# Kernel optimization log

Hardware: AMD Instinct MI355X
Metric: run time of the kernel (lower is better)

Reference implementation:

```python
import jax, jax.numpy as jnp
import numpy as np

# SMPL-style skeleton: parent index per joint (parent < child, root = -1)
PARENTS = [-1, 0, 0, 0, 1, 2, 3, 4, 5, 6, 7, 8, 9, 9, 9, 12, 13, 14, 16, 17, 18, 19, 20, 21]
END_SITES = [10, 11, 15, 22, 23]  # feet, head, hands
NUM_JOINTS = len(PARENTS)


def rot6d_to_matrix(x):
    """6D rotation rep -> 3x3 matrix via Gram-Schmidt. x: [..., 6] -> [..., 3, 3].
    eye(3).reshape(-1)[:6] = [1,0,0,0,1,0] maps to identity under this (row-stacked) convention."""
    a1, a2 = x[..., 0:3], x[..., 3:6]
    b1 = a1 / jnp.linalg.norm(a1, axis=-1, keepdims=True)
    a2p = a2 - jnp.sum(b1 * a2, axis=-1, keepdims=True) * b1
    b2 = a2p / jnp.linalg.norm(a2p, axis=-1, keepdims=True)
    b3 = jnp.cross(b1, b2)
    return jnp.stack([b1, b2, b3], axis=-2)


def fk_positions(rot, offsets):
    """Forward kinematics (faithful to _recompute_joint_global_info).
    rot: [F, J, 3, 3] local joint rotations; offsets: [F, J, 3].
    Returns global joint positions [F, J, 3]. Loop is over the fixed, small
    joint hierarchy (structural), fully vectorized over frames."""
    positions = [offsets[:, 0]]          # root: offset only
    orientations = [rot[:, 0]]           # root: local rotation
    for i in range(1, NUM_JOINTS):
        pi = PARENTS[i]
        po = orientations[pi]            # [F, 3, 3]
        pos = jnp.einsum('fab,fb->fa', po, offsets[:, i]) + positions[pi]
        positions.append(pos)
        orientations.append(po @ rot[:, i])
    return jnp.stack(positions, axis=1)  # [F, J, 3]


def setup_inputs() -> dict:
    key = jax.random.key(0)
    ks = jax.random.split(key, 6)
    F = 65536
    return {
        'poseA': jax.random.normal(ks[0], (F, NUM_JOINTS, 6), dtype=jnp.float32),
        'poseB': jax.random.normal(ks[1], (F, NUM_JOINTS, 6), dtype=jnp.float32),
        'joint_offsets_A': jax.random.normal(ks[2], (F, NUM_JOINTS, 3), dtype=jnp.float32),
        'joint_offsets_B': jax.random.normal(ks[3], (F, NUM_JOINTS, 3), dtype=jnp.float32),
        't_poseA': jax.random.normal(ks[4], (NUM_JOINTS, 3), dtype=jnp.float32),
        't_poseB': jax.random.normal(ks[5], (NUM_JOINTS, 3), dtype=jnp.float32),
    }


def reference(poseA, poseB, joint_offsets_A, joint_offsets_B, t_poseA, t_poseB):
    ee = jnp.array(END_SITES)
    # 6D -> rotation matrices (to_matrix)
    RA = rot6d_to_matrix(poseA)
    RB = rot6d_to_matrix(poseB)
    # sequential per-joint FK (the hot loop)
    posA = fk_positions(RA, joint_offsets_A)
    posB = fk_positions(RB, joint_offsets_B)
    # bbox scale from T-pose
    scale_A = jnp.max(t_poseA, axis=0) - jnp.min(t_poseA, axis=0)  # [3]
    scale_B = jnp.max(t_poseB, axis=0) - jnp.min(t_poseB, axis=0)
    eeA = posA[:, ee, :] - t_poseA[ee, :]   # [F, E, 3]
    eeB = posB[:, ee, :] - t_poseB[ee, :]
    loss = jnp.mean((eeA / scale_A - eeB / scale_B) ** 2)
    return loss
```

## Files before the change

kernel.cpp:

```cpp
#include <hip/hip_runtime.h>


struct V3 { float x, y, z; };
struct M3 { float m[3][3]; };
struct FK { M3 o; V3 p; };

__device__ __forceinline__ V3 matvec(const M3& A, const V3& v) {
    return { A.m[0][0]*v.x + A.m[0][1]*v.y + A.m[0][2]*v.z,
             A.m[1][0]*v.x + A.m[1][1]*v.y + A.m[1][2]*v.z,
             A.m[2][0]*v.x + A.m[2][1]*v.y + A.m[2][2]*v.z };
}

__device__ __forceinline__ M3 matmul(const M3& A, const M3& B) {
    M3 C;
#pragma unroll
    for (int i = 0; i < 3; i++)
#pragma unroll
        for (int j = 0; j < 3; j++)
            C.m[i][j] = A.m[i][0]*B.m[0][j] + A.m[i][1]*B.m[1][j] + A.m[i][2]*B.m[2][j];
    return C;
}

__device__ __forceinline__ M3 rot6d(float v0, float v1, float v2,
                                    float v3, float v4, float v5) {
    float n1 = v0*v0 + v1*v1 + v2*v2;
    float r1 = 1.0f / sqrtf(n1);
    V3 b1 = { v0*r1, v1*r1, v2*r1 };
    float d = b1.x*v3 + b1.y*v4 + b1.z*v5;
    V3 u = { v3 - d*b1.x, v4 - d*b1.y, v5 - d*b1.z };
    float n2 = u.x*u.x + u.y*u.y + u.z*u.z;
    float r2 = 1.0f / sqrtf(n2);
    V3 b2 = { u.x*r2, u.y*r2, u.z*r2 };
    V3 b3 = { b1.y*b2.z - b1.z*b2.y, b1.z*b2.x - b1.x*b2.z, b1.x*b2.y - b1.y*b2.x };
    M3 R;
    R.m[0][0]=b1.x; R.m[0][1]=b1.y; R.m[0][2]=b1.z;
    R.m[1][0]=b2.x; R.m[1][1]=b2.y; R.m[1][2]=b2.z;
    R.m[2][0]=b3.x; R.m[2][1]=b3.y; R.m[2][2]=b3.z;
    return R;
}

__device__ __forceinline__ FK fk_step(float a0,float a1,float a2,float a3,float a4,float a5,
                                      float ox,float oy,float oz, const FK& par) {
    V3 t = matvec(par.o, {ox, oy, oz});
    FK s;
    s.p = { par.p.x + t.x, par.p.y + t.y, par.p.z + t.z };
    s.o = matmul(par.o, rot6d(a0, a1, a2, a3, a4, a5));
    return s;
}

__device__ __forceinline__ V3 fk_end(float ox, float oy, float oz, const FK& par) {
    V3 t = matvec(par.o, {ox, oy, oz});
    return { par.p.x + t.x, par.p.y + t.y, par.p.z + t.z };
}

#define GLDS16(gp, lp) __builtin_amdgcn_global_load_lds( \
    (const __attribute__((address_space(1))) void*)(gp), \
    (__attribute__((address_space(3))) void*)(lp), 16, 0, 0)

#define VWAIT(n) do { asm volatile("s_waitcnt vmcnt(" #n ")" ::: "memory"); \
                      __builtin_amdgcn_sched_barrier(0); } while (0)
#define LWAIT0()  do { asm volatile("s_waitcnt lgkmcnt(0)" ::: "memory"); \
                      __builtin_amdgcn_sched_barrier(0); } while (0)

__device__ __forceinline__ void stage(const float* __restrict__ P,
                                      const float* __restrict__ O,
                                      const int* pOfs, const int* oOfs,
                                      float4* pbuf, float4* obuf, int st) {
#pragma unroll
    for (int k = 0; k < 6; k++)
        GLDS16(P + st*24 + pOfs[k], pbuf + 64*k);
#pragma unroll
    for (int k = 0; k < 3; k++)
        GLDS16(O + st*12 + oOfs[k], obuf + 64*k);
}

#define READQ(pb, ob) \
    q0 = (pb)[0]; q1 = (pb)[1]; q2 = (pb)[2]; q3 = (pb)[3]; q4 = (pb)[4]; q5 = (pb)[5]; \
    r0 = (ob)[0]; r1 = (ob)[1]; r2 = (ob)[2];
#define J0ROT  q0.x,q0.y,q0.z,q0.w,q1.x,q1.y
#define J1ROT  q1.z,q1.w,q2.x,q2.y,q2.z,q2.w
#define J2ROT  q3.x,q3.y,q3.z,q3.w,q4.x,q4.y
#define J3ROT  q4.z,q4.w,q5.x,q5.y,q5.z,q5.w
#define J0OFF  r0.x,r0.y,r0.z
#define J1OFF  r0.w,r1.x,r1.y
#define J2OFF  r1.z,r1.w,r2.x
#define J3OFF  r2.y,r2.z,r2.w

__global__ __launch_bounds__(128)
void ee_loss_kernel(const float* __restrict__ poseA, const float* __restrict__ poseB,
                    const float* __restrict__ offA,  const float* __restrict__ offB,
                    const float* __restrict__ tA,    const float* __restrict__ tB,
                    float* __restrict__ out, float inv_count) {
    __shared__ float4 s_pose[2][2][64*6];
    __shared__ float4 s_off [2][2][64*3];
    __shared__ float s_inv[6];
    __shared__ float s_d[15];
    float* s_eeB = (float*)&s_off[0][0][0];

    const int tid  = threadIdx.x;
    const int wid  = tid >> 6;
    const int lane = tid & 63;
    const bool isB = wid & 1;
    const long long f0 = (long long)blockIdx.x * 64;

    const float* __restrict__ P = (isB ? poseB : poseA) + f0 * 144;
    const float* __restrict__ O = (isB ? offB  : offA ) + f0 * 72;

    float4* pb0 = &s_pose[wid][0][0];
    float4* pb1 = &s_pose[wid][1][0];
    float4* ob0 = &s_off[wid][0][0];
    float4* ob1 = &s_off[wid][1][0];
    const float4* rp0 = pb0 + lane * 6;
    const float4* rp1 = pb1 + lane * 6;
    const float4* ro0 = ob0 + lane * 3;
    const float4* ro1 = ob1 + lane * 3;

    if (tid < 6) {
        const float* tp = (tid < 3) ? tA : tB;
        int ax = (tid < 3) ? tid : tid - 3;
        float mn = tp[ax], mx = mn;
#pragma unroll
        for (int j = 1; j < 24; j++) {
            float v = tp[j*3 + ax];
            mn = fminf(mn, v); mx = fmaxf(mx, v);
        }
        s_inv[tid] = 1.0f / (mx - mn);
    }
    if (tid < 15) {
        const int EE[5] = {10, 11, 15, 22, 23};
        int e = tid / 3, ax = tid - 3*e;
        int j = EE[e];
        float mnA = tA[ax], mxA = mnA, mnB = tB[ax], mxB = mnB;
#pragma unroll
        for (int k = 1; k < 24; k++) {
            float a = tA[k*3 + ax], b = tB[k*3 + ax];
            mnA = fminf(mnA, a); mxA = fmaxf(mxA, a);
            mnB = fminf(mnB, b); mxB = fmaxf(mxB, b);
        }
        s_d[tid] = tB[j*3 + ax]/(mxB - mnB) - tA[j*3 + ax]/(mxA - mnA);
    }

    int pOfs[6], oOfs[3];
#pragma unroll
    for (int k = 0; k < 6; k++) {
        int idx = lane + 64*k, f = idx/6, c = idx - 6*f;
        pOfs[k] = f*144 + c*4;
    }
#pragma unroll
    for (int k = 0; k < 3; k++) {
        int idx = lane + 64*k, f = idx/3, c = idx - 3*f;
        oOfs[k] = f*72 + c*4;
    }

    stage(P, O, pOfs, oOfs, pb0, ob0, 0);
    stage(P, O, pOfs, oOfs, pb1, ob1, 1);

    float4 q0, q1, q2, q3, q4, q5, r0, r1, r2;

    VWAIT(9);
    READQ(rp0, ro0);
    LWAIT0();
    stage(P, O, pOfs, oOfs, pb0, ob0, 2);
    FK s0; s0.o = rot6d(J0ROT); s0.p = { r0.x, r0.y, r0.z };
    FK s1 = fk_step(J1ROT, J1OFF, s0);
    FK s2 = fk_step(J2ROT, J2OFF, s0);
    FK s3 = fk_step(J3ROT, J3OFF, s0);

    VWAIT(9);
    READQ(rp1, ro1);
    LWAIT0();
    stage(P, O, pOfs, oOfs, pb1, ob1, 3);
    FK s4 = fk_step(J0ROT, J0OFF, s1);
    FK s5 = fk_step(J1ROT, J1OFF, s2);
    FK s6 = fk_step(J2ROT, J2OFF, s3);
    FK s7 = fk_step(J3ROT, J3OFF, s4);

    VWAIT(9);
    READQ(rp0, ro0);
    LWAIT0();
    stage(P, O, pOfs, oOfs, pb0, ob0, 4);
    FK s8 = fk_step(J0ROT, J0OFF, s5);
    FK s9 = fk_step(J1ROT, J1OFF, s6);
    V3 e10 = fk_end(J2OFF, s7);
    V3 e11 = fk_end(J3OFF, s8);

    VWAIT(9);
    READQ(rp1, ro1);
    LWAIT0();
    stage(P, O, pOfs, oOfs, pb1, ob1, 5);
    FK s12 = fk_step(J0ROT, J0OFF, s9);
    FK s13 = fk_step(J1ROT, J1OFF, s9);
    FK s14 = fk_step(J2ROT, J2OFF, s9);
    V3 e15 = fk_end(J3OFF, s12);

    VWAIT(9);
    READQ(rp0, ro0);
    FK s16 = fk_step(J0ROT, J0OFF, s13);
    FK s17 = fk_step(J1ROT, J1OFF, s14);
    FK s18 = fk_step(J2ROT, J2OFF, s16);
    FK s19 = fk_step(J3ROT, J3OFF, s17);

    VWAIT(0);
    READQ(rp1, ro1);
    FK s20 = fk_step(J0ROT, J0OFF, s18);
    FK s21 = fk_step(J1ROT, J1OFF, s19);
    V3 e22 = fk_end(J2OFF, s20);
    V3 e23 = fk_end(J3OFF, s21);

    __syncthreads();
    if (isB) {
        float* eb = s_eeB + lane * 15;
        eb[ 0] = e10.x; eb[ 1] = e10.y; eb[ 2] = e10.z;
        eb[ 3] = e11.x; eb[ 4] = e11.y; eb[ 5] = e11.z;
        eb[ 6] = e15.x; eb[ 7] = e15.y; eb[ 8] = e15.z;
        eb[ 9] = e22.x; eb[10] = e22.y; eb[11] = e22.z;
        eb[12] = e23.x; eb[13] = e23.y; eb[14] = e23.z;
    }
    __syncthreads();

    if (!isB) {
        const float iax = s_inv[0], iay = s_inv[1], iaz = s_inv[2];
        const float ibx = s_inv[3], iby = s_inv[4], ibz = s_inv[5];
        const float* eb = s_eeB + lane * 15;
        float t0  = e10.x*iax - eb[ 0]*ibx + s_d[ 0];
        float t1  = e10.y*iay - eb[ 1]*iby + s_d[ 1];
        float t2  = e10.z*iaz - eb[ 2]*ibz + s_d[ 2];
        float t3  = e11.x*iax - eb[ 3]*ibx + s_d[ 3];
        float t4  = e11.y*iay - eb[ 4]*iby + s_d[ 4];
        float t5  = e11.z*iaz - eb[ 5]*ibz + s_d[ 5];
        float t6  = e15.x*iax - eb[ 6]*ibx + s_d[ 6];
        float t7  = e15.y*iay - eb[ 7]*iby + s_d[ 7];
        float t8  = e15.z*iaz - eb[ 8]*ibz + s_d[ 8];
        float t9  = e22.x*iax - eb[ 9]*ibx + s_d[ 9];
        float t10 = e22.y*iay - eb[10]*iby + s_d[10];
        float t11 = e22.z*iaz - eb[11]*ibz + s_d[11];
        float t12 = e23.x*iax - eb[12]*ibx + s_d[12];
        float t13 = e23.y*iay - eb[13]*iby + s_d[13];
        float t14 = e23.z*iaz - eb[14]*ibz + s_d[14];
        float local = ((t0*t0 + t1*t1) + (t2*t2 + t3*t3) + (t4*t4 + t5*t5) +
                       (t6*t6 + t7*t7) + (t8*t8 + t9*t9) + (t10*t10 + t11*t11) +
                       (t12*t12 + t13*t13) + t14*t14) * inv_count;
#pragma unroll
        for (int off = 32; off > 0; off >>= 1)
            local += __shfl_down(local, off, 64);
        if (lane == 0) atomicAdd(out, local);
    }
}

extern "C" void kernel_launch(void* const* d_in, const int* in_sizes, int n_in,
                              void* d_out, int out_size, void* d_ws, size_t ws_size,
                              hipStream_t stream) {
    const float* poseA = (const float*)d_in[0];
    const float* poseB = (const float*)d_in[1];
    const float* offA  = (const float*)d_in[2];
    const float* offB  = (const float*)d_in[3];
    const float* tA    = (const float*)d_in[4];
    const float* tB    = (const float*)d_in[5];
    float* out = (float*)d_out;

    const int F = in_sizes[0] / 144;
    const int blocks = F / 64;
    const float inv_count = 1.0f / ((float)F * 15.0f);

    hipMemsetAsync(out, 0, sizeof(float), stream);
    ee_loss_kernel<<<blocks, 128, 0, stream>>>(poseA, poseB, offA, offB, tA, tB,
                                               out, inv_count);
}
```

Measured before the change: 149.9 us.

## Pack A and B frames into one wave, exchange end-effectors via cross-half shuffle

Restructures the kernel so each 64-lane wave processes 32 frames, with the lower half computing skeleton A and the upper half skeleton B, instead of a 128-thread block with one wave per skeleton. The shared-memory round-trip and two __syncthreads used to combine A and B end-effectors are replaced by __shfl_xor across the wave halves. LDS reads are split into smaller groups interleaved with the FK steps to cut register pressure and overlap LDS latency. The price is twice as many blocks, half-wave-interleaved LDS layouts, and more waitcnt points. Half of each wave also sits idle during the loss arithmetic.

```diff
diff --git a/kernel.cpp b/kernel.cpp
--- a/kernel.cpp
+++ b/kernel.cpp
@@ -62,21 +62,24 @@
 #define LWAIT0()  do { asm volatile("s_waitcnt lgkmcnt(0)" ::: "memory"); \
                       __builtin_amdgcn_sched_barrier(0); } while (0)
 
-__device__ __forceinline__ void stage(const float* __restrict__ P,
-                                      const float* __restrict__ O,
-                                      const int* pOfs, const int* oOfs,
-                                      float4* pbuf, float4* obuf, int st) {
-#pragma unroll
-    for (int k = 0; k < 6; k++)
-        GLDS16(P + st*24 + pOfs[k], pbuf + 64*k);
-#pragma unroll
-    for (int k = 0; k < 3; k++)
-        GLDS16(O + st*12 + oOfs[k], obuf + 64*k);
-}
-
-#define READQ(pb, ob) \
-    q0 = (pb)[0]; q1 = (pb)[1]; q2 = (pb)[2]; q3 = (pb)[3]; q4 = (pb)[4]; q5 = (pb)[5]; \
-    r0 = (ob)[0]; r1 = (ob)[1]; r2 = (ob)[2];
+#define STAGE(B, ST) do { \
+    GLDS16(psrc[0] + (ST)*24, &s_pose[B][  0]); \
+    GLDS16(psrc[1] + (ST)*24, &s_pose[B][ 64]); \
+    GLDS16(psrc[2] + (ST)*24, &s_pose[B][128]); \
+    GLDS16(psrc[3] + (ST)*24, &s_pose[B][192]); \
+    GLDS16(psrc[4] + (ST)*24, &s_pose[B][256]); \
+    GLDS16(psrc[5] + (ST)*24, &s_pose[B][320]); \
+    GLDS16(osrc[0] + (ST)*12, &s_off [B][  0]); \
+    GLDS16(osrc[1] + (ST)*12, &s_off [B][ 64]); \
+    GLDS16(osrc[2] + (ST)*12, &s_off [B][128]); \
+} while (0)
+
+#define RG1(B)  q0 = s_pose[B][ps[0]]; q1 = s_pose[B][ps[1]]; q2 = s_pose[B][ps[2]]; \
+                r0 = s_off[B][os3[0]]; r1 = s_off[B][os3[1]];
+#define RQ35(B) q3 = s_pose[B][ps[3]]; q4 = s_pose[B][ps[4]]; q5 = s_pose[B][ps[5]];
+#define RQ34(B) q3 = s_pose[B][ps[3]]; q4 = s_pose[B][ps[4]];
+#define RR2(B)  r2 = s_off[B][os3[2]];
+
 #define J0ROT  q0.x,q0.y,q0.z,q0.w,q1.x,q1.y
 #define J1ROT  q1.z,q1.w,q2.x,q2.y,q2.z,q2.w
 #define J2ROT  q3.x,q3.y,q3.z,q3.w,q4.x,q4.y
@@ -86,49 +89,38 @@
 #define J2OFF  r1.z,r1.w,r2.x
 #define J3OFF  r2.y,r2.z,r2.w
 
-__global__ __launch_bounds__(128)
+__global__ __launch_bounds__(64, 2)
 void ee_loss_kernel(const float* __restrict__ poseA, const float* __restrict__ poseB,
                     const float* __restrict__ offA,  const float* __restrict__ offB,
                     const float* __restrict__ tA,    const float* __restrict__ tB,
                     float* __restrict__ out, float inv_count) {
-    __shared__ float4 s_pose[2][2][64*6];
-    __shared__ float4 s_off [2][2][64*3];
+    __shared__ float4 s_pose[2][384];
+    __shared__ float4 s_off [2][192];
     __shared__ float s_inv[6];
     __shared__ float s_d[15];
-    float* s_eeB = (float*)&s_off[0][0][0];
-
-    const int tid  = threadIdx.x;
-    const int wid  = tid >> 6;
-    const int lane = tid & 63;
-    const bool isB = wid & 1;
-    const long long f0 = (long long)blockIdx.x * 64;
-
-    const float* __restrict__ P = (isB ? poseB : poseA) + f0 * 144;
-    const float* __restrict__ O = (isB ? offB  : offA ) + f0 * 72;
-
-    float4* pb0 = &s_pose[wid][0][0];
-    float4* pb1 = &s_pose[wid][1][0];
-    float4* ob0 = &s_off[wid][0][0];
-    float4* ob1 = &s_off[wid][1][0];
-    const float4* rp0 = pb0 + lane * 6;
-    const float4* rp1 = pb1 + lane * 6;
-    const float4* ro0 = ob0 + lane * 3;
-    const float4* ro1 = ob1 + lane * 3;
-
-    if (tid < 6) {
-        const float* tp = (tid < 3) ? tA : tB;
-        int ax = (tid < 3) ? tid : tid - 3;
+
+    const int lane = threadIdx.x;
+    const int h    = lane >> 5;
+    const int l5   = lane & 31;
+    const long long f0 = (long long)blockIdx.x * 32;
+
+    const float* P = (h ? poseB : poseA) + f0 * 144;
+    const float* O = (h ? offB  : offA ) + f0 * 72;
+
+    if (lane < 6) {
+        const float* tp = (lane < 3) ? tA : tB;
+        int ax = (lane < 3) ? lane : lane - 3;
         float mn = tp[ax], mx = mn;
 #pragma unroll
         for (int j = 1; j < 24; j++) {
             float v = tp[j*3 + ax];
             mn = fminf(mn, v); mx = fmaxf(mx, v);
         }
-        s_inv[tid] = 1.0f / (mx - mn);
-    }
-    if (tid < 15) {
+        s_inv[lane] = 1.0f / (mx - mn);
+    }
+    if (lane < 15) {
         const int EE[5] = {10, 11, 15, 22, 23};
-        int e = tid / 3, ax = tid - 3*e;
+        int e = lane / 3, ax = lane - 3*e;
         int j = EE[e];
         float mnA = tA[ax], mxA = mnA, mnB = tB[ax], mxB = mnB;
 #pragma unroll
@@ -137,114 +129,135 @@
             mnA = fminf(mnA, a); mxA = fmaxf(mxA, a);
             mnB = fminf(mnB, b); mxB = fmaxf(mxB, b);
         }
-        s_d[tid] = tB[j*3 + ax]/(mxB - mnB) - tA[j*3 + ax]/(mxA - mnA);
-    }
-
-    int pOfs[6], oOfs[3];
+        s_d[lane] = tB[j*3 + ax]/(mxB - mnB) - tA[j*3 + ax]/(mxA - mnA);
+    }
+    __builtin_amdgcn_sched_barrier(0);
+
+    const float* psrc[6];
 #pragma unroll
     for (int k = 0; k < 6; k++) {
-        int idx = lane + 64*k, f = idx/6, c = idx - 6*f;
-        pOfs[k] = f*144 + c*4;
-    }
+        int idx = l5 + 32*k, f = idx/6, c = idx - 6*f;
+        psrc[k] = P + f*144 + c*4;
+    }
+    const float* osrc[3];
 #pragma unroll
     for (int k = 0; k < 3; k++) {
-        int idx = lane + 64*k, f = idx/3, c = idx - 3*f;
-        oOfs[k] = f*72 + c*4;
-    }
-
-    stage(P, O, pOfs, oOfs, pb0, ob0, 0);
-    stage(P, O, pOfs, oOfs, pb1, ob1, 1);
+        int idx = l5 + 32*k, f = idx/3, c = idx - 3*f;
+        osrc[k] = O + f*72 + c*4;
+    }
+
+    int ps[6], os3[3];
+#pragma unroll
+    for (int c = 0; c < 6; c++) {
+        int idx = 6*l5 + c;
+        ps[c] = ((idx >> 5) << 6) + (h << 5) + (idx & 31);
+    }
+#pragma unroll
+    for (int c = 0; c < 3; c++) {
+        int idx = 3*l5 + c;
+        os3[c] = ((idx >> 5) << 6) + (h << 5) + (idx & 31);
+    }
+
+    STAGE(0, 0);
+    STAGE(1, 1);
 
     float4 q0, q1, q2, q3, q4, q5, r0, r1, r2;
 
     VWAIT(9);
-    READQ(rp0, ro0);
-    LWAIT0();
-    stage(P, O, pOfs, oOfs, pb0, ob0, 2);
+    RG1(0); LWAIT0();
     FK s0; s0.o = rot6d(J0ROT); s0.p = { r0.x, r0.y, r0.z };
     FK s1 = fk_step(J1ROT, J1OFF, s0);
+    RQ35(0); RR2(0); LWAIT0();
+    STAGE(0, 2);
     FK s2 = fk_step(J2ROT, J2OFF, s0);
     FK s3 = fk_step(J3ROT, J3OFF, s0);
 
     VWAIT(9);
-    READQ(rp1, ro1);
-    LWAIT0();
-    stage(P, O, pOfs, oOfs, pb1, ob1, 3);
+    RG1(1); LWAIT0();
     FK s4 = fk_step(J0ROT, J0OFF, s1);
     FK s5 = fk_step(J1ROT, J1OFF, s2);
+    RQ35(1); RR2(1); LWAIT0();
+    STAGE(1, 3);
     FK s6 = fk_step(J2ROT, J2OFF, s3);
     FK s7 = fk_step(J3ROT, J3OFF, s4);
 
     VWAIT(9);
-    READQ(rp0, ro0);
-    LWAIT0();
-    stage(P, O, pOfs, oOfs, pb0, ob0, 4);
+    RG1(0); LWAIT0();
     FK s8 = fk_step(J0ROT, J0OFF, s5);
     FK s9 = fk_step(J1ROT, J1OFF, s6);
+    RR2(0); LWAIT0();
+    STAGE(0, 4);
     V3 e10 = fk_end(J2OFF, s7);
     V3 e11 = fk_end(J3OFF, s8);
 
     VWAIT(9);
-    READQ(rp1, ro1);
-    LWAIT0();
-    stage(P, O, pOfs, oOfs, pb1, ob1, 5);
+    RG1(1); LWAIT0();
     FK s12 = fk_step(J0ROT, J0OFF, s9);
     FK s13 = fk_step(J1ROT, J1OFF, s9);
+    RQ34(1); RR2(1); LWAIT0();
+    STAGE(1, 5);
     FK s14 = fk_step(J2ROT, J2OFF, s9);
     V3 e15 = fk_end(J3OFF, s12);
 
     VWAIT(9);
-    READQ(rp0, ro0);
+    RG1(0); LWAIT0();
     FK s16 = fk_step(J0ROT, J0OFF, s13);
     FK s17 = fk_step(J1ROT, J1OFF, s14);
+    RQ35(0); RR2(0); LWAIT0();
     FK s18 = fk_step(J2ROT, J2OFF, s16);
     FK s19 = fk_step(J3ROT, J3OFF, s17);
 
     VWAIT(0);
-    READQ(rp1, ro1);
+    RG1(1); LWAIT0();
     FK s20 = fk_step(J0ROT, J0OFF, s18);
     FK s21 = fk_step(J1ROT, J1OFF, s19);
+    RR2(1); LWAIT0();
     V3 e22 = fk_end(J2OFF, s20);
     V3 e23 = fk_end(J3OFF, s21);
 
-    __syncthreads();
-    if (isB) {
-        float* eb = s_eeB + lane * 15;
-        eb[ 0] = e10.x; eb[ 1] = e10.y; eb[ 2] = e10.z;
-        eb[ 3] = e11.x; eb[ 4] = e11.y; eb[ 5] = e11.z;
-        eb[ 6] = e15.x; eb[ 7] = e15.y; eb[ 8] = e15.z;
-        eb[ 9] = e22.x; eb[10] = e22.y; eb[11] = e22.z;
-        eb[12] = e23.x; eb[13] = e23.y; eb[14] = e23.z;
-    }
-    __syncthreads();
-
-    if (!isB) {
+    float p0  = __shfl_xor(e10.x, 32, 64);
+    float p1  = __shfl_xor(e10.y, 32, 64);
+    float p2  = __shfl_xor(e10.z, 32, 64);
+    float p3  = __shfl_xor(e11.x, 32, 64);
+    float p4  = __shfl_xor(e11.y, 32, 64);
+    float p5  = __shfl_xor(e11.z, 32, 64);
+    float p6  = __shfl_xor(e15.x, 32, 64);
+    float p7  = __shfl_xor(e15.y, 32, 64);
+    float p8  = __shfl_xor(e15.z, 32, 64);
+    float p9  = __shfl_xor(e22.x, 32, 64);
+    float p10 = __shfl_xor(e22.y, 32, 64);
+    float p11 = __shfl_xor(e22.z, 32, 64);
+    float p12 = __shfl_xor(e23.x, 32, 64);
+    float p13 = __shfl_xor(e23.y, 32, 64);
+    float p14 = __shfl_xor(e23.z, 32, 64);
+
+    float local = 0.0f;
+    if (h == 0) {
         const float iax = s_inv[0], iay = s_inv[1], iaz = s_inv[2];
         const float ibx = s_inv[3], iby = s_inv[4], ibz = s_inv[5];
-        const float* eb = s_eeB + lane * 15;
-        float t0  = e10.x*iax - eb[ 0]*ibx + s_d[ 0];
-        float t1  = e10.y*iay - eb[ 1]*iby + s_d[ 1];
-        float t2  = e10.z*iaz - eb[ 2]*ibz + s_d[ 2];
-        float t3  = e11.x*iax - eb[ 3]*ibx + s_d[ 3];
-        float t4  = e11.y*iay - eb[ 4]*iby + s_d[ 4];
-        float t5  = e11.z*iaz - eb[ 5]*ibz + s_d[ 5];
-        float t6  = e15.x*iax - eb[ 6]*ibx + s_d[ 6];
-        float t7  = e15.y*iay - eb[ 7]*iby + s_d[ 7];
-        float t8  = e15.z*iaz - eb[ 8]*ibz + s_d[ 8];
-        float t9  = e22.x*iax - eb[ 9]*ibx + s_d[ 9];
-        float t10 = e22.y*iay - eb[10]*iby + s_d[10];
-        float t11 = e22.z*iaz - eb[11]*ibz + s_d[11];
-        float t12 = e23.x*iax - eb[12]*ibx + s_d[12];
-        float t13 = e23.y*iay - eb[13]*iby + s_d[13];
-        float t14 = e23.z*iaz - eb[14]*ibz + s_d[14];
-        float local = ((t0*t0 + t1*t1) + (t2*t2 + t3*t3) + (t4*t4 + t5*t5) +
-                       (t6*t6 + t7*t7) + (t8*t8 + t9*t9) + (t10*t10 + t11*t11) +
-                       (t12*t12 + t13*t13) + t14*t14) * inv_count;
-#pragma unroll
-        for (int off = 32; off > 0; off >>= 1)
-            local += __shfl_down(local, off, 64);
-        if (lane == 0) atomicAdd(out, local);
-    }
+        float t0  = e10.x*iax - p0 *ibx + s_d[ 0];
+        float t1  = e10.y*iay - p1 *iby + s_d[ 1];
+        float t2  = e10.z*iaz - p2 *ibz + s_d[ 2];
+        float t3  = e11.x*iax - p3 *ibx + s_d[ 3];
+        float t4  = e11.y*iay - p4 *iby + s_d[ 4];
+        float t5  = e11.z*iaz - p5 *ibz + s_d[ 5];
+        float t6  = e15.x*iax - p6 *ibx + s_d[ 6];
+        float t7  = e15.y*iay - p7 *iby + s_d[ 7];
+        float t8  = e15.z*iaz - p8 *ibz + s_d[ 8];
+        float t9  = e22.x*iax - p9 *ibx + s_d[ 9];
+        float t10 = e22.y*iay - p10*iby + s_d[10];
+        float t11 = e22.z*iaz - p11*ibz + s_d[11];
+        float t12 = e23.x*iax - p12*ibx + s_d[12];
+        float t13 = e23.y*iay - p13*iby + s_d[13];
+        float t14 = e23.z*iaz - p14*ibz + s_d[14];
+        local = ((t0*t0 + t1*t1) + (t2*t2 + t3*t3) + (t4*t4 + t5*t5) +
+                 (t6*t6 + t7*t7) + (t8*t8 + t9*t9) + (t10*t10 + t11*t11) +
+                 (t12*t12 + t13*t13) + t14*t14) * inv_count;
+    }
+#pragma unroll
+    for (int off = 32; off > 0; off >>= 1)
+        local += __shfl_down(local, off, 64);
+    if (lane == 0) atomicAdd(out, local);
 }
 
 extern "C" void kernel_launch(void* const* d_in, const int* in_sizes, int n_in,
@@ -259,10 +272,10 @@
     float* out = (float*)d_out;
 
     const int F = in_sizes[0] / 144;
-    const int blocks = F / 64;
+    const int blocks = F / 32;
     const float inv_count = 1.0f / ((float)F * 15.0f);
 
     hipMemsetAsync(out, 0, sizeof(float), stream);
-    ee_loss_kernel<<<blocks, 128, 0, stream>>>(poseA, poseB, offA, offB, tA, tB,
-                                               out, inv_count);
-}
+    ee_loss_kernel<<<blocks, 64, 0, stream>>>(poseA, poseB, offA, offB, tA, tB,
+                                              out, inv_count);
+}
```

New measurement: 162.7 us. 8.5% more time.
